# Kernel tuning notes

Hardware: AMD Instinct MI355X
Metric: run time of the kernel (lower is better)

## Reference

```python
import jax, jax.numpy as jnp
import numpy as np

NG = 100000   # num gene nodes
ND = 100000   # num disease nodes
E = 400000    # edges per edge type
EL = 200000   # label edges
C = 128       # hidden_channels


def segment_softmax(logits, seg, n):
    # PyG-style softmax over segments (numerically stable, eps=1e-16)
    m = jax.ops.segment_max(logits, seg, num_segments=n)
    e = jnp.exp(logits - m[seg])
    s = jax.ops.segment_sum(e, seg, num_segments=n)
    return e / (s[seg] + 1e-16)


def hgat_edge_type(x_src, x_dst, src_idx, dst_idx, edge_emb, wi, wj, we, att_b, n_dst):
    # gather (message), per-edge attention logit = [x_i|x_j|e] @ w  (split to avoid concat)
    x_i = x_dst[dst_idx]                                   # [E, C]
    x_j = x_src[src_idx]                                   # [E, C]
    logit = x_i @ wi + x_j @ wj + edge_emb @ we + att_b    # [E, 1] (num_heads=1)
    alpha = jax.nn.leaky_relu(logit, 0.2)
    alpha = segment_softmax(alpha, dst_idx, n_dst)
    out = jax.ops.segment_sum(x_i * alpha, dst_idx, num_segments=n_dst)  # scatter-add
    return jax.nn.relu(out)


def setup_inputs() -> dict:
    key = jax.random.key(0)
    ks = jax.random.split(key, 24)
    s = 0.02
    return {
        "x_gene": jax.random.normal(ks[0], (NG, C), jnp.float32),
        "x_disease": jax.random.normal(ks[1], (ND, C), jnp.float32),
        "edge_index_g2d": jnp.stack([jax.random.randint(ks[2], (E,), 0, NG),
                                     jax.random.randint(ks[3], (E,), 0, ND)]),
        "edge_index_d2g": jnp.stack([jax.random.randint(ks[4], (E,), 0, ND),
                                     jax.random.randint(ks[5], (E,), 0, NG)]),
        "edge_emb_g2d": jax.random.normal(ks[6], (E, C), jnp.float32),
        "edge_emb_d2g": jax.random.normal(ks[7], (E, C), jnp.float32),
        "edge_label_index": jnp.stack([jax.random.randint(ks[8], (EL,), 0, NG),
                                       jax.random.randint(ks[9], (EL,), 0, ND)]),
        # HeteroDictLinear node / edge weights (stored [in, out])
        "Wn_gene": jax.random.normal(ks[10], (C, C), jnp.float32) * s,
        "bn_gene": jnp.zeros((C,), jnp.float32),
        "Wn_disease": jax.random.normal(ks[11], (C, C), jnp.float32) * s,
        "bn_disease": jnp.zeros((C,), jnp.float32),
        "We_g2d": jax.random.normal(ks[12], (C, C), jnp.float32) * s,
        "be_g2d": jnp.zeros((C,), jnp.float32),
        "We_d2g": jax.random.normal(ks[13], (C, C), jnp.float32) * s,
        "be_d2g": jnp.zeros((C,), jnp.float32),
        # attention head: Linear(3*C, 1) applied to cat([x_i, x_j, edge_emb])
        "att_w": jax.random.normal(ks[14], (3 * C, 1), jnp.float32) * s,
        "att_b": jnp.zeros((1,), jnp.float32),
        # decoder
        "W1": jax.random.normal(ks[15], (2 * C, C), jnp.float32) * s,
        "b1": jnp.zeros((C,), jnp.float32),
        "W2": jax.random.normal(ks[16], (C, 1), jnp.float32) * s,
        "b2": jnp.zeros((1,), jnp.float32),
    }


def reference(x_gene, x_disease, edge_index_g2d, edge_index_d2g, edge_emb_g2d,
              edge_emb_d2g, edge_label_index, Wn_gene, bn_gene, Wn_disease,
              bn_disease, We_g2d, be_g2d, We_d2g, be_d2g, att_w, att_b,
              W1, b1, W2, b2):
    # per-type node / edge linear projections
    x_g = x_gene @ Wn_gene + bn_gene
    x_d = x_disease @ Wn_disease + bn_disease
    e_g2d = edge_emb_g2d @ We_g2d + be_g2d
    e_d2g = edge_emb_d2g @ We_d2g + be_d2g
    wi, wj, we = att_w[:C], att_w[C:2 * C], att_w[2 * C:]
    # gene->disease aggregates into disease nodes; disease->gene into gene nodes
    z_disease = hgat_edge_type(x_g, x_d, edge_index_g2d[0], edge_index_g2d[1],
                               e_g2d, wi, wj, we, att_b, ND)
    z_gene = hgat_edge_type(x_d, x_g, edge_index_d2g[0], edge_index_d2g[1],
                            e_d2g, wi, wj, we, att_b, NG)
    # decoder on label edges
    row, col = edge_label_index[0], edge_label_index[1]
    z = jnp.concatenate([z_gene[row], z_disease[col]], axis=-1)  # [EL, 2C]
    h = jax.nn.relu(z @ W1 + b1)
    pred = (h @ W2 + b2).reshape(-1)                             # [EL]
    return pred, z_gene, z_disease
```

## Files before the change

kernel.cpp:

```cpp
#include <hip/hip_runtime.h>
#include <hip/hip_bf16.h>
#include <stdint.h>

#define NGn 100000
#define NDn 100000
#define NEn 400000
#define ELn 200000

typedef __bf16 bf16x8 __attribute__((ext_vector_type(8)));
typedef float  f32x4  __attribute__((ext_vector_type(4)));

__device__ __forceinline__ bf16x8 cvt8(const float* __restrict__ f) {
    f32x4 a = *(const f32x4*)f;
    f32x4 b = *(const f32x4*)(f + 4);
    bf16x8 r;
    r[0] = (__bf16)a[0]; r[1] = (__bf16)a[1]; r[2] = (__bf16)a[2]; r[3] = (__bf16)a[3];
    r[4] = (__bf16)b[0]; r[5] = (__bf16)b[1]; r[6] = (__bf16)b[2]; r[7] = (__bf16)b[3];
    return r;
}

__global__ void scatter_mask(const int* __restrict__ g2d_dst,
                             const int* __restrict__ d2g_dst,
                             uint8_t* __restrict__ mask_d,
                             uint8_t* __restrict__ mask_g, int n) {
    int i = blockIdx.x * blockDim.x + threadIdx.x;
    if (i < n) {
        mask_d[g2d_dst[i]] = 1;
        mask_g[d2g_dst[i]] = 1;
    }
}

__global__ __launch_bounds__(256) void node_gemm(
    const float* __restrict__ X, const float* __restrict__ W,
    const float* __restrict__ bias, const uint8_t* __restrict__ mask,
    float* __restrict__ Zf, __bf16* __restrict__ Zb, int Nrows)
{
    __shared__ __bf16 Wt[128 * 136];
    const int tid = threadIdx.x;
    for (int idx = tid; idx < 128 * 128; idx += 256) {
        int k = idx >> 7, c = idx & 127;
        Wt[c * 136 + k] = (__bf16)W[idx];
    }
    __syncthreads();

    const int wave = tid >> 6;
    const int lane = tid & 63;
    const int m = lane & 15;
    const int q = lane >> 4;

    float bcol[8];
#pragma unroll
    for (int nt = 0; nt < 8; ++nt) bcol[nt] = bias[nt * 16 + m];

    const int ntiles = (Nrows + 63) >> 6;
    for (int t = blockIdx.x; t < ntiles; t += gridDim.x) {
        const int base = t * 64;
        const int row_a = base + wave * 16 + m;
        const int rowa_c = row_a < Nrows ? row_a : (Nrows - 1);

        f32x4 acc[8];
#pragma unroll
        for (int nt = 0; nt < 8; ++nt) acc[nt] = f32x4{0.f, 0.f, 0.f, 0.f};

#pragma unroll
        for (int kk = 0; kk < 4; ++kk) {
            bf16x8 a = cvt8(X + (size_t)rowa_c * 128 + kk * 32 + q * 8);
#pragma unroll
            for (int nt = 0; nt < 8; ++nt) {
                bf16x8 b = *(const bf16x8*)(&Wt[(nt * 16 + m) * 136 + kk * 32 + q * 8]);
                acc[nt] = __builtin_amdgcn_mfma_f32_16x16x32_bf16(a, b, acc[nt], 0, 0, 0);
            }
        }

#pragma unroll
        for (int reg = 0; reg < 4; ++reg) {
            int r = base + wave * 16 + q * 4 + reg;
            if (r < Nrows) {
                float mk = mask[r] ? 1.f : 0.f;
#pragma unroll
                for (int nt = 0; nt < 8; ++nt) {
                    float v = acc[nt][reg] + bcol[nt];
                    v = (v > 0.f ? v : 0.f) * mk;
                    Zf[(size_t)r * 128 + nt * 16 + m] = v;
                    if (Zb) Zb[(size_t)r * 128 + nt * 16 + m] = (__bf16)v;
                }
            }
        }
    }
}

__global__ __launch_bounds__(256) void h_gemm(
    const __bf16* __restrict__ Zgb, const __bf16* __restrict__ Zdb,
    const float* __restrict__ W1,
    __bf16* __restrict__ Hgb, __bf16* __restrict__ Hdb)
{
    __shared__ __bf16 Wt[128 * 136];
    const int half = gridDim.x >> 1;
    const bool gene = (int)blockIdx.x < half;
    const __bf16* __restrict__ Z = gene ? Zgb : Zdb;
    __bf16*       __restrict__ H = gene ? Hgb : Hdb;
    const float*  __restrict__ Ws = W1 + (gene ? 0 : 128 * 128);

    const int tid = threadIdx.x;
    for (int idx = tid; idx < 128 * 128; idx += 256) {
        int k = idx >> 7, c = idx & 127;
        Wt[c * 136 + k] = (__bf16)Ws[idx];
    }
    __syncthreads();

    const int wave = tid >> 6;
    const int lane = tid & 63;
    const int m = lane & 15;
    const int q = lane >> 4;

    const int ntiles = (NGn + 63) >> 6;
    const int b0 = gene ? (int)blockIdx.x : (int)blockIdx.x - half;
    for (int t = b0; t < ntiles; t += half) {
        const int base = t * 64;
        const int row_a = base + wave * 16 + m;
        const int rowa_c = row_a < NGn ? row_a : (NGn - 1);

        f32x4 acc[8];
#pragma unroll
        for (int nt = 0; nt < 8; ++nt) acc[nt] = f32x4{0.f, 0.f, 0.f, 0.f};

#pragma unroll
        for (int kk = 0; kk < 4; ++kk) {
            bf16x8 a = *(const bf16x8*)(Z + (size_t)rowa_c * 128 + kk * 32 + q * 8);
#pragma unroll
            for (int nt = 0; nt < 8; ++nt) {
                bf16x8 b = *(const bf16x8*)(&Wt[(nt * 16 + m) * 136 + kk * 32 + q * 8]);
                acc[nt] = __builtin_amdgcn_mfma_f32_16x16x32_bf16(a, b, acc[nt], 0, 0, 0);
            }
        }

#pragma unroll
        for (int reg = 0; reg < 4; ++reg) {
            int r = base + wave * 16 + q * 4 + reg;
            if (r < NGn) {
#pragma unroll
                for (int nt = 0; nt < 8; ++nt)
                    H[(size_t)r * 128 + nt * 16 + m] = (__bf16)acc[nt][reg];
            }
        }
    }
}

__global__ __launch_bounds__(256) void edge_mlp(
    const __bf16* __restrict__ Hgb, const __bf16* __restrict__ Hdb,
    const int* __restrict__ eli, const float* __restrict__ b1,
    const float* __restrict__ W2, const float* __restrict__ b2,
    float* __restrict__ pred)
{
    const int tid = threadIdx.x;
    const int wave = tid >> 6;
    const int lane = tid & 63;
    const int l16 = lane & 15;
    const int sub = lane >> 4;

    float b1c[8], w2c[8];
#pragma unroll
    for (int j = 0; j < 8; ++j) {
        b1c[j] = b1[l16 * 8 + j];
        w2c[j] = W2[l16 * 8 + j];
    }
    const float bb = b2[0];

    const int nunits = ELn >> 3;
    const int wid0 = (int)blockIdx.x * 4 + wave;
    const int wstride = (int)gridDim.x * 4;
    for (int u = wid0; u < nunits; u += wstride) {
        const int e0 = u * 8 + sub * 2;
        const int g0 = eli[e0],       g1 = eli[e0 + 1];
        const int d0 = eli[ELn + e0], d1 = eli[ELn + e0 + 1];

        bf16x8 vg0 = *(const bf16x8*)(Hgb + (size_t)g0 * 128 + l16 * 8);
        bf16x8 vd0 = *(const bf16x8*)(Hdb + (size_t)d0 * 128 + l16 * 8);
        bf16x8 vg1 = *(const bf16x8*)(Hgb + (size_t)g1 * 128 + l16 * 8);
        bf16x8 vd1 = *(const bf16x8*)(Hdb + (size_t)d1 * 128 + l16 * 8);

        float s0 = 0.f, s1 = 0.f;
#pragma unroll
        for (int j = 0; j < 8; ++j) {
            float h0 = (float)vg0[j] + (float)vd0[j] + b1c[j];
            float h1 = (float)vg1[j] + (float)vd1[j] + b1c[j];
            h0 = h0 > 0.f ? h0 : 0.f;
            h1 = h1 > 0.f ? h1 : 0.f;
            s0 += h0 * w2c[j];
            s1 += h1 * w2c[j];
        }
#pragma unroll
        for (int off = 1; off < 16; off <<= 1) {
            s0 += __shfl_xor(s0, off, 64);
            s1 += __shfl_xor(s1, off, 64);
        }
        if (l16 == 0) {
            pred[e0]     = s0 + bb;
            pred[e0 + 1] = s1 + bb;
        }
    }
}

__global__ __launch_bounds__(256) void mlp_kernel(
    const __bf16* __restrict__ zgb, const __bf16* __restrict__ zdb,
    const float* __restrict__ zgf, const float* __restrict__ zdf,
    int usebf, const int* __restrict__ eli,
    const float* __restrict__ W1, const float* __restrict__ b1,
    const float* __restrict__ W2, const float* __restrict__ b2,
    float* __restrict__ pred)
{
    __shared__ __bf16 Wt[128 * 256];
    const int tid = threadIdx.x;
    for (int idx = tid; idx < 256 * 128; idx += 256) {
        int k = idx >> 7, c = idx & 127;
        int kc = k >> 3, kl = k & 7;
        Wt[c * 256 + ((kc ^ (c & 7)) * 8 + kl)] = (__bf16)W1[idx];
    }
    __syncthreads();

    const int wave = tid >> 6;
    const int lane = tid & 63;
    const int m = lane & 15;
    const int q = lane >> 4;

    float b1c[8], w2c[8];
#pragma unroll
    for (int nt = 0; nt < 8; ++nt) {
        b1c[nt] = b1[nt * 16 + m];
        w2c[nt] = W2[nt * 16 + m];
    }
    const float bb = b2[0];

    const int ngroups = ELn / 64;
    for (int g = blockIdx.x; g < ngroups; g += gridDim.x) {
        const int e = g * 64 + wave * 16 + m;
        const int grow = eli[e];
        const int dcol = eli[ELn + e];

        f32x4 acc[8];
#pragma unroll
        for (int nt = 0; nt < 8; ++nt) acc[nt] = f32x4{0.f, 0.f, 0.f, 0.f};

#pragma unroll
        for (int kk = 0; kk < 8; ++kk) {
            bf16x8 a;
            if (usebf) {
                const __bf16* src = (kk < 4) ? (zgb + (size_t)grow * 128 + kk * 32)
                                             : (zdb + (size_t)dcol * 128 + (kk - 4) * 32);
                a = *(const bf16x8*)(src + q * 8);
            } else {
                const float* src = (kk < 4) ? (zgf + (size_t)grow * 128 + kk * 32)
                                            : (zdf + (size_t)dcol * 128 + (kk - 4) * 32);
                a = cvt8(src + q * 8);
            }
            const int kcr = kk * 4 + q;
#pragma unroll
            for (int nt = 0; nt < 8; ++nt) {
                int n = nt * 16 + m;
                bf16x8 b = *(const bf16x8*)(&Wt[n * 256 + ((kcr ^ (n & 7)) * 8)]);
                acc[nt] = __builtin_amdgcn_mfma_f32_16x16x32_bf16(a, b, acc[nt], 0, 0, 0);
            }
        }

        float pb[4];
#pragma unroll
        for (int reg = 0; reg < 4; ++reg) {
            float s = 0.f;
#pragma unroll
            for (int nt = 0; nt < 8; ++nt) {
                float h = acc[nt][reg] + b1c[nt];
                h = h > 0.f ? h : 0.f;
                s += h * w2c[nt];
            }
            pb[reg] = s;
        }
#pragma unroll
        for (int off = 1; off < 16; off <<= 1) {
#pragma unroll
            for (int reg = 0; reg < 4; ++reg)
                pb[reg] += __shfl_xor(pb[reg], off, 64);
        }
        if (m == 0) {
#pragma unroll
            for (int reg = 0; reg < 4; ++reg) {
                int er = g * 64 + wave * 16 + q * 4 + reg;
                pred[er] = pb[reg] + bb;
            }
        }
    }
}

extern "C" void kernel_launch(void* const* d_in, const int* in_sizes, int n_in,
                              void* d_out, int out_size, void* d_ws, size_t ws_size,
                              hipStream_t stream) {
    const float* x_gene    = (const float*)d_in[0];
    const float* x_disease = (const float*)d_in[1];
    const int*   ei_g2d    = (const int*)d_in[2];
    const int*   ei_d2g    = (const int*)d_in[3];
    const int*   eli       = (const int*)d_in[6];
    const float* Wn_gene   = (const float*)d_in[7];
    const float* bn_gene   = (const float*)d_in[8];
    const float* Wn_dis    = (const float*)d_in[9];
    const float* bn_dis    = (const float*)d_in[10];
    const float* W1        = (const float*)d_in[17];
    const float* b1        = (const float*)d_in[18];
    const float* W2        = (const float*)d_in[19];
    const float* b2        = (const float*)d_in[20];

    float* out   = (float*)d_out;
    float* predp = out;
    float* zgf   = out + ELn;
    float* zdf   = zgf + (size_t)NGn * 128;

    uint8_t* mask_d = (uint8_t*)d_ws;
    uint8_t* mask_g = mask_d + NDn;

    const size_t zelems = (size_t)NGn * 128;
    const size_t mirror_off = 200704;
    const bool   mirror2 = ws_size >= mirror_off + 2 * zelems * sizeof(__bf16);
    const bool   mirror4 = ws_size >= mirror_off + 4 * zelems * sizeof(__bf16);
    __bf16* zgb = mirror2 ? (__bf16*)((char*)d_ws + mirror_off) : nullptr;
    __bf16* zdb = mirror2 ? zgb + zelems : nullptr;
    __bf16* Hgb = mirror4 ? zdb + zelems : nullptr;
    __bf16* Hdb = mirror4 ? Hgb + zelems : nullptr;

    hipMemsetAsync(d_ws, 0, NGn + NDn, stream);
    scatter_mask<<<(NEn + 255) / 256, 256, 0, stream>>>(
        ei_g2d + NEn, ei_d2g + NEn, mask_d, mask_g, NEn);

    node_gemm<<<1024, 256, 0, stream>>>(x_gene, Wn_gene, bn_gene, mask_g, zgf, zgb, NGn);
    node_gemm<<<1024, 256, 0, stream>>>(x_disease, Wn_dis, bn_dis, mask_d, zdf, zdb, NDn);

    if (mirror4) {
        h_gemm<<<2048, 256, 0, stream>>>(zgb, zdb, W1, Hgb, Hdb);
        edge_mlp<<<2048, 256, 0, stream>>>(Hgb, Hdb, eli, b1, W2, b2, predp);
    } else {
        mlp_kernel<<<512, 256, 0, stream>>>(zgb, zdb, zgf, zdf, mirror2 ? 1 : 0,
                                            eli, W1, b1, W2, b2, predp);
    }
}
```

Measured before the change: 525.0 us.

## Fuse node projection and decoder W1 GEMM into one kernel via LDS staging

Merges the per-type node GEMM and the decoder's first-layer projection (H = Z @ W1 half) into a single kernel. Each wave stages its 16-row Z tile in swizzled shared memory and runs the second MFMA GEMM directly, so the bf16 Z mirror is no longer written to or re-read from global memory, and one launch is removed. Shared-memory weight layouts switch from padded to XOR-swizzled. The trade-offs are higher LDS usage (about 80KB per block), which can lower occupancy, and extra block-wide barriers per tile.

```diff
diff --git a/kernel.cpp b/kernel.cpp
--- a/kernel.cpp
+++ b/kernel.cpp
@@ -17,6 +17,10 @@
     r[0] = (__bf16)a[0]; r[1] = (__bf16)a[1]; r[2] = (__bf16)a[2]; r[3] = (__bf16)a[3];
     r[4] = (__bf16)b[0]; r[5] = (__bf16)b[1]; r[6] = (__bf16)b[2]; r[7] = (__bf16)b[3];
     return r;
+}
+
+__device__ __forceinline__ int swz(int row, int col) {
+    return row * 128 + ((((col >> 3) ^ (row & 7)) << 3) | (col & 7));
 }
 
 __global__ void scatter_mask(const int* __restrict__ g2d_dst,
@@ -30,16 +34,34 @@
     }
 }
 
-__global__ __launch_bounds__(256) void node_gemm(
-    const float* __restrict__ X, const float* __restrict__ W,
-    const float* __restrict__ bias, const uint8_t* __restrict__ mask,
-    float* __restrict__ Zf, __bf16* __restrict__ Zb, int Nrows)
+__global__ __launch_bounds__(256) void fused_node_h(
+    const float* __restrict__ Xg, const float* __restrict__ Wng,
+    const float* __restrict__ bng, const uint8_t* __restrict__ mg,
+    float* __restrict__ Zgf, __bf16* __restrict__ Hgb,
+    const float* __restrict__ Xd, const float* __restrict__ Wnd,
+    const float* __restrict__ bnd, const uint8_t* __restrict__ md,
+    float* __restrict__ Zdf, __bf16* __restrict__ Hdb,
+    const float* __restrict__ W1)
 {
-    __shared__ __bf16 Wt[128 * 136];
+    __shared__ __bf16 WnT[128 * 128];
+    __shared__ __bf16 W1T[128 * 128];
+    __shared__ __bf16 zt[4][16 * 128];
+
+    const int half = gridDim.x >> 1;
+    const bool gene = (int)blockIdx.x < half;
+    const float*   __restrict__ X    = gene ? Xg : Xd;
+    const float*   __restrict__ Wn   = gene ? Wng : Wnd;
+    const float*   __restrict__ bv   = gene ? bng : bnd;
+    const uint8_t* __restrict__ mask = gene ? mg : md;
+    float*  __restrict__ Zf = gene ? Zgf : Zdf;
+    __bf16* __restrict__ H  = gene ? Hgb : Hdb;
+    const float* __restrict__ W1s = W1 + (gene ? 0 : 128 * 128);
+
     const int tid = threadIdx.x;
     for (int idx = tid; idx < 128 * 128; idx += 256) {
         int k = idx >> 7, c = idx & 127;
-        Wt[c * 136 + k] = (__bf16)W[idx];
+        WnT[swz(c, k)] = (__bf16)Wn[idx];
+        W1T[swz(c, k)] = (__bf16)W1s[idx];
     }
     __syncthreads();
 
@@ -47,71 +69,11 @@
     const int lane = tid & 63;
     const int m = lane & 15;
     const int q = lane >> 4;
+    __bf16* zw = zt[wave];
 
     float bcol[8];
 #pragma unroll
-    for (int nt = 0; nt < 8; ++nt) bcol[nt] = bias[nt * 16 + m];
-
-    const int ntiles = (Nrows + 63) >> 6;
-    for (int t = blockIdx.x; t < ntiles; t += gridDim.x) {
-        const int base = t * 64;
-        const int row_a = base + wave * 16 + m;
-        const int rowa_c = row_a < Nrows ? row_a : (Nrows - 1);
-
-        f32x4 acc[8];
-#pragma unroll
-        for (int nt = 0; nt < 8; ++nt) acc[nt] = f32x4{0.f, 0.f, 0.f, 0.f};
-
-#pragma unroll
-        for (int kk = 0; kk < 4; ++kk) {
-            bf16x8 a = cvt8(X + (size_t)rowa_c * 128 + kk * 32 + q * 8);
-#pragma unroll
-            for (int nt = 0; nt < 8; ++nt) {
-                bf16x8 b = *(const bf16x8*)(&Wt[(nt * 16 + m) * 136 + kk * 32 + q * 8]);
-                acc[nt] = __builtin_amdgcn_mfma_f32_16x16x32_bf16(a, b, acc[nt], 0, 0, 0);
-            }
-        }
-
-#pragma unroll
-        for (int reg = 0; reg < 4; ++reg) {
-            int r = base + wave * 16 + q * 4 + reg;
-            if (r < Nrows) {
-                float mk = mask[r] ? 1.f : 0.f;
-#pragma unroll
-                for (int nt = 0; nt < 8; ++nt) {
-                    float v = acc[nt][reg] + bcol[nt];
-                    v = (v > 0.f ? v : 0.f) * mk;
-                    Zf[(size_t)r * 128 + nt * 16 + m] = v;
-                    if (Zb) Zb[(size_t)r * 128 + nt * 16 + m] = (__bf16)v;
-                }
-            }
-        }
-    }
-}
-
-__global__ __launch_bounds__(256) void h_gemm(
-    const __bf16* __restrict__ Zgb, const __bf16* __restrict__ Zdb,
-    const float* __restrict__ W1,
-    __bf16* __restrict__ Hgb, __bf16* __restrict__ Hdb)
-{
-    __shared__ __bf16 Wt[128 * 136];
-    const int half = gridDim.x >> 1;
-    const bool gene = (int)blockIdx.x < half;
-    const __bf16* __restrict__ Z = gene ? Zgb : Zdb;
-    __bf16*       __restrict__ H = gene ? Hgb : Hdb;
-    const float*  __restrict__ Ws = W1 + (gene ? 0 : 128 * 128);
-
-    const int tid = threadIdx.x;
-    for (int idx = tid; idx < 128 * 128; idx += 256) {
-        int k = idx >> 7, c = idx & 127;
-        Wt[c * 136 + k] = (__bf16)Ws[idx];
-    }
-    __syncthreads();
-
-    const int wave = tid >> 6;
-    const int lane = tid & 63;
-    const int m = lane & 15;
-    const int q = lane >> 4;
+    for (int nt = 0; nt < 8; ++nt) bcol[nt] = bv[nt * 16 + m];
 
     const int ntiles = (NGn + 63) >> 6;
     const int b0 = gene ? (int)blockIdx.x : (int)blockIdx.x - half;
@@ -126,23 +88,54 @@
 
 #pragma unroll
         for (int kk = 0; kk < 4; ++kk) {
-            bf16x8 a = *(const bf16x8*)(Z + (size_t)rowa_c * 128 + kk * 32 + q * 8);
-#pragma unroll
-            for (int nt = 0; nt < 8; ++nt) {
-                bf16x8 b = *(const bf16x8*)(&Wt[(nt * 16 + m) * 136 + kk * 32 + q * 8]);
+            bf16x8 a = cvt8(X + (size_t)rowa_c * 128 + kk * 32 + q * 8);
+#pragma unroll
+            for (int nt = 0; nt < 8; ++nt) {
+                bf16x8 b = *(const bf16x8*)(&WnT[swz(nt * 16 + m, kk * 32 + q * 8)]);
                 acc[nt] = __builtin_amdgcn_mfma_f32_16x16x32_bf16(a, b, acc[nt], 0, 0, 0);
             }
         }
 
 #pragma unroll
         for (int reg = 0; reg < 4; ++reg) {
-            int r = base + wave * 16 + q * 4 + reg;
+            const int rr = q * 4 + reg;
+            const int r  = base + wave * 16 + rr;
+            const bool ok = r < NGn;
+            const float mk = (ok && mask[ok ? r : 0]) ? 1.f : 0.f;
+#pragma unroll
+            for (int nt = 0; nt < 8; ++nt) {
+                float v = acc[nt][reg] + bcol[nt];
+                v = (v > 0.f ? v : 0.f) * mk;
+                if (ok) Zf[(size_t)r * 128 + nt * 16 + m] = v;
+                zw[swz(rr, nt * 16 + m)] = (__bf16)v;
+            }
+        }
+        __syncthreads();
+
+        f32x4 acc2[8];
+#pragma unroll
+        for (int nt = 0; nt < 8; ++nt) acc2[nt] = f32x4{0.f, 0.f, 0.f, 0.f};
+
+#pragma unroll
+        for (int kk = 0; kk < 4; ++kk) {
+            bf16x8 a2 = *(const bf16x8*)(&zw[swz(m, kk * 32 + q * 8)]);
+#pragma unroll
+            for (int nt = 0; nt < 8; ++nt) {
+                bf16x8 b2 = *(const bf16x8*)(&W1T[swz(nt * 16 + m, kk * 32 + q * 8)]);
+                acc2[nt] = __builtin_amdgcn_mfma_f32_16x16x32_bf16(a2, b2, acc2[nt], 0, 0, 0);
+            }
+        }
+
+#pragma unroll
+        for (int reg = 0; reg < 4; ++reg) {
+            const int r = base + wave * 16 + q * 4 + reg;
             if (r < NGn) {
 #pragma unroll
                 for (int nt = 0; nt < 8; ++nt)
-                    H[(size_t)r * 128 + nt * 16 + m] = (__bf16)acc[nt][reg];
-            }
-        }
+                    H[(size_t)r * 128 + nt * 16 + m] = (__bf16)acc2[nt][reg];
+            }
+        }
+        __syncthreads();
     }
 }
 
@@ -201,10 +194,67 @@
     }
 }
 
+__global__ __launch_bounds__(256) void node_gemm(
+    const float* __restrict__ X, const float* __restrict__ W,
+    const float* __restrict__ bias, const uint8_t* __restrict__ mask,
+    float* __restrict__ Zf, int Nrows)
+{
+    __shared__ __bf16 Wt[128 * 136];
+    const int tid = threadIdx.x;
+    for (int idx = tid; idx < 128 * 128; idx += 256) {
+        int k = idx >> 7, c = idx & 127;
+        Wt[c * 136 + k] = (__bf16)W[idx];
+    }
+    __syncthreads();
+
+    const int wave = tid >> 6;
+    const int lane = tid & 63;
+    const int m = lane & 15;
+    const int q = lane >> 4;
+
+    float bcol[8];
+#pragma unroll
+    for (int nt = 0; nt < 8; ++nt) bcol[nt] = bias[nt * 16 + m];
+
+    const int ntiles = (Nrows + 63) >> 6;
+    for (int t = blockIdx.x; t < ntiles; t += gridDim.x) {
+        const int base = t * 64;
+        const int row_a = base + wave * 16 + m;
+        const int rowa_c = row_a < Nrows ? row_a : (Nrows - 1);
+
+        f32x4 acc[8];
+#pragma unroll
+        for (int nt = 0; nt < 8; ++nt) acc[nt] = f32x4{0.f, 0.f, 0.f, 0.f};
+
+#pragma unroll
+        for (int kk = 0; kk < 4; ++kk) {
+            bf16x8 a = cvt8(X + (size_t)rowa_c * 128 + kk * 32 + q * 8);
+#pragma unroll
+            for (int nt = 0; nt < 8; ++nt) {
+                bf16x8 b = *(const bf16x8*)(&Wt[(nt * 16 + m) * 136 + kk * 32 + q * 8]);
+                acc[nt] = __builtin_amdgcn_mfma_f32_16x16x32_bf16(a, b, acc[nt], 0, 0, 0);
+            }
+        }
+
+#pragma unroll
+        for (int reg = 0; reg < 4; ++reg) {
+            int r = base + wave * 16 + q * 4 + reg;
+            if (r < Nrows) {
+                float mk = mask[r] ? 1.f : 0.f;
+#pragma unroll
+                for (int nt = 0; nt < 8; ++nt) {
+                    float v = acc[nt][reg] + bcol[nt];
+                    v = (v > 0.f ? v : 0.f) * mk;
+                    Zf[(size_t)r * 128 + nt * 16 + m] = v;
+                }
+            }
+        }
+    }
+}
+
 __global__ __launch_bounds__(256) void mlp_kernel(
-    const __bf16* __restrict__ zgb, const __bf16* __restrict__ zdb,
     const float* __restrict__ zgf, const float* __restrict__ zdf,
-    int usebf, const int* __restrict__ eli,
+    const int* __restrict__ eli,
     const float* __restrict__ W1, const float* __restrict__ b1,
     const float* __restrict__ W2, const float* __restrict__ b2,
     float* __restrict__ pred)
@@ -243,16 +293,9 @@
 
 #pragma unroll
         for (int kk = 0; kk < 8; ++kk) {
-            bf16x8 a;
-            if (usebf) {
-                const __bf16* src = (kk < 4) ? (zgb + (size_t)grow * 128 + kk * 32)
-                                             : (zdb + (size_t)dcol * 128 + (kk - 4) * 32);
-                a = *(const bf16x8*)(src + q * 8);
-            } else {
-                const float* src = (kk < 4) ? (zgf + (size_t)grow * 128 + kk * 32)
-                                            : (zdf + (size_t)dcol * 128 + (kk - 4) * 32);
-                a = cvt8(src + q * 8);
-            }
+            const float* src = (kk < 4) ? (zgf + (size_t)grow * 128 + kk * 32)
+                                        : (zdf + (size_t)dcol * 128 + (kk - 4) * 32);
+            bf16x8 a = cvt8(src + q * 8);
             const int kcr = kk * 4 + q;
 #pragma unroll
             for (int nt = 0; nt < 8; ++nt) {
@@ -315,27 +358,24 @@
     uint8_t* mask_d = (uint8_t*)d_ws;
     uint8_t* mask_g = mask_d + NDn;
 
-    const size_t zelems = (size_t)NGn * 128;
+    const size_t helems = (size_t)NGn * 128;
     const size_t mirror_off = 200704;
-    const bool   mirror2 = ws_size >= mirror_off + 2 * zelems * sizeof(__bf16);
-    const bool   mirror4 = ws_size >= mirror_off + 4 * zelems * sizeof(__bf16);
-    __bf16* zgb = mirror2 ? (__bf16*)((char*)d_ws + mirror_off) : nullptr;
-    __bf16* zdb = mirror2 ? zgb + zelems : nullptr;
-    __bf16* Hgb = mirror4 ? zdb + zelems : nullptr;
-    __bf16* Hdb = mirror4 ? Hgb + zelems : nullptr;
+    const bool   mirrorH = ws_size >= mirror_off + 2 * helems * sizeof(__bf16);
+    __bf16* Hgb = mirrorH ? (__bf16*)((char*)d_ws + mirror_off) : nullptr;
+    __bf16* Hdb = mirrorH ? Hgb + helems : nullptr;
 
     hipMemsetAsync(d_ws, 0, NGn + NDn, stream);
     scatter_mask<<<(NEn + 255) / 256, 256, 0, stream>>>(
         ei_g2d + NEn, ei_d2g + NEn, mask_d, mask_g, NEn);
 
-    node_gemm<<<1024, 256, 0, stream>>>(x_gene, Wn_gene, bn_gene, mask_g, zgf, zgb, NGn);
-    node_gemm<<<1024, 256, 0, stream>>>(x_disease, Wn_dis, bn_dis, mask_d, zdf, zdb, NDn);
-
-    if (mirror4) {
-        h_gemm<<<2048, 256, 0, stream>>>(zgb, zdb, W1, Hgb, Hdb);
+    if (mirrorH) {
+        fused_node_h<<<1024, 256, 0, stream>>>(
+            x_gene, Wn_gene, bn_gene, mask_g, zgf, Hgb,
+            x_disease, Wn_dis, bn_dis, mask_d, zdf, Hdb, W1);
         edge_mlp<<<2048, 256, 0, stream>>>(Hgb, Hdb, eli, b1, W2, b2, predp);
     } else {
-        mlp_kernel<<<512, 256, 0, stream>>>(zgb, zdb, zgf, zdf, mirror2 ? 1 : 0,
-                                            eli, W1, b1, W2, b2, predp);
-    }
-}
+        node_gemm<<<1024, 256, 0, stream>>>(x_gene, Wn_gene, bn_gene, mask_g, zgf, NGn);
+        node_gemm<<<1024, 256, 0, stream>>>(x_disease, Wn_dis, bn_dis, mask_d, zdf, NDn);
+        mlp_kernel<<<512, 256, 0, stream>>>(zgf, zdf, eli, W1, b1, W2, b2, predp);
+    }
+}
```

New measurement: 499.3 us. 4.9% less time.
